# Optimization experiments

Hardware: AMD Instinct MI355X
Metric: run time of the kernel (lower is better)

## Reference

```python
import jax, jax.numpy as jnp
import numpy as np

B, N, A, H, MID = 256, 128, 15, 32, 256  # batch, nodes(=in_channels), actions, EQL-proxy hidden, critic mid_weight


def _glorot(k, shape):
    lim = float(np.sqrt(6.0 / (shape[0] + shape[1])))
    return jax.random.uniform(k, shape, jnp.float32, -lim, lim)


def setup_inputs() -> dict:
    key = jax.random.key(0)
    ks = jax.random.split(key, 10)
    obs = jax.random.normal(ks[0], (B, N), jnp.float32)
    return dict(
        obs=obs,
        # messenger EQL proxy: 4 -> H -> 1
        mw1=_glorot(ks[1], (4, H)), mb1=jnp.zeros((H,), jnp.float32),
        mw2=_glorot(ks[2], (H, 1)), mb2=jnp.zeros((1,), jnp.float32),
        # actor EQL proxy: 3 -> H -> 1
        aw1=_glorot(ks[3], (3, H)), ab1=jnp.zeros((H,), jnp.float32),
        aw2=_glorot(ks[4], (H, 1)), ab2=jnp.zeros((1,), jnp.float32),
        # critic MLP: N -> MID -> MID -> MID -> 1 (depth=4)
        cw1=_glorot(ks[5], (N, MID)), cb1=jnp.zeros((MID,), jnp.float32),
        cw2=_glorot(ks[6], (MID, MID)), cb2=jnp.zeros((MID,), jnp.float32),
        cw3=_glorot(ks[7], (MID, MID)), cb3=jnp.zeros((MID,), jnp.float32),
        cw4=_glorot(ks[8], (MID, 1)), cb4=jnp.zeros((1,), jnp.float32),
    )


def reference(obs, mw1, mb1, mw2, mb2, aw1, ab1, aw2, ab2,
              cw1, cb1, cw2, cb2, cw3, cb3, cw4, cb4):
    b, n = obs.shape
    coor = jnp.arange(n, dtype=jnp.float32) / n  # append_index coordinate channel
    x = jnp.stack([obs, jnp.broadcast_to(coor, obs.shape)], axis=-1)  # [B,n,2]

    # all-pairs message pass: msg_in[b,i,j] = concat(x[b,i], x[b,j])  -> [B,n,n,4]
    xi = jnp.broadcast_to(x[:, :, None, :], (b, n, n, 2))
    xj = jnp.broadcast_to(x[:, None, :, :], (b, n, n, 2))
    msg_in = jnp.concatenate([xi, xj], axis=-1)
    messages = jax.nn.relu(msg_in @ mw1 + mb1) @ mw2 + mb2  # [B,n,n,1]
    msg = jnp.sum(messages, axis=-2)[..., 0]  # sum over j, squeeze -> [B,n]

    # append_index again on the aggregated messages
    m = jnp.stack([msg, jnp.broadcast_to(coor, msg.shape)], axis=-1)  # [B,n,2]

    # node x action cross: am[b,i,a] = concat(m[b,i], a)  -> [B,n,A,3]
    acts = jnp.arange(A, dtype=jnp.float32)[None, None, :, None]
    mi = jnp.broadcast_to(m[:, :, None, :], (b, n, A, 2))
    aj = jnp.broadcast_to(acts, (b, n, A, 1))
    am = jnp.concatenate([mi, aj], axis=-1)
    am_messages = jax.nn.relu(am @ aw1 + ab1) @ aw2 + ab2  # [B,n,A,1]
    logits = jnp.sum(am_messages, axis=-3)[..., 0]  # sum over nodes (obs_dim=-3) -> [B,A]

    # critic MLP on raw obs
    h = jax.nn.relu(obs @ cw1 + cb1)
    h = jax.nn.relu(h @ cw2 + cb2)
    h = jax.nn.relu(h @ cw3 + cb3)
    value = h @ cw4 + cb4  # [B,1]
    return logits, value
```

## Files before the change

kernel.cpp:

```cpp
#include <hip/hip_runtime.h>

#define BB    256
#define NN    128
#define AA    15
#define HH    32
#define MIDD  256
#define NCRIT 16

typedef _Float16 h2_t  __attribute__((ext_vector_type(2)));
typedef _Float16 f16x8 __attribute__((ext_vector_type(8)));
typedef float    f32x4 __attribute__((ext_vector_type(4)));

struct MsgS {
    _Float16 vh[NN][HH];
    float4   p4[8][NN];
    float    part[4][16][8];
};
struct CriS {
    _Float16 hA[2][16][264];
};

__global__ __launch_bounds__(512, 4) void gacq_v13(
    const float* __restrict__ obs,
    const float* __restrict__ mw1, const float* __restrict__ mb1,
    const float* __restrict__ mw2, const float* __restrict__ mb2,
    const float* __restrict__ aw1, const float* __restrict__ ab1,
    const float* __restrict__ aw2, const float* __restrict__ ab2,
    const float* __restrict__ cw1, const float* __restrict__ cb1,
    const float* __restrict__ cw2, const float* __restrict__ cb2,
    const float* __restrict__ cw3, const float* __restrict__ cb3,
    const float* __restrict__ cw4, const float* __restrict__ cb4,
    float* __restrict__ out)
{
    __shared__ __align__(16) float aux_s[356];
    __shared__ __align__(16) float obs_s[NN];
    __shared__ __align__(16) union { MsgS m; CriS c; } u_s;

    const int blk  = blockIdx.x;
    const int t    = threadIdx.x;
    const int lane = t & 63;

    if (blk >= NCRIT) {
        const int b = blk - NCRIT;

        if (t < NN) obs_s[t] = obs[b * NN + t];
        if (t < 354) {
            float v;
            if      (t < 128) v = mw1[t];
            else if (t < 224) v = aw1[t - 128];
            else if (t < 256) v = ab1[t - 224];
            else if (t < 288) v = aw2[t - 256];
            else if (t < 320) v = mw2[t - 288];
            else if (t < 352) v = mb1[t - 320];
            else if (t == 352) v = mb2[0];
            else               v = ab2[0];
            aux_s[t] = v;
        }
        __syncthreads();

        for (int e = t; e < NN * HH / 2; e += 512) {
            const int   j  = e >> 4, kp = e & 15;
            const int   k0 = kp * 2;
            const float cj = (float)j * (1.0f / (float)NN);
            const float v0 = obs_s[j] * aux_s[64 + k0]     + cj * aux_s[96 + k0]     + aux_s[320 + k0];
            const float v1 = obs_s[j] * aux_s[64 + k0 + 1] + cj * aux_s[96 + k0 + 1] + aux_s[320 + k0 + 1];
            h2_t p; p[0] = (_Float16)v0; p[1] = (_Float16)v1;
            *(h2_t*)&u_s.m.vh[j][k0] = p;
        }

        const int kg = t & 7;
        const int rg = (t >> 3) & 15;
        const int jg = t >> 7;

        h2_t u2[8][2], w2h[2];
        w2h[0][0] = (_Float16)aux_s[288 + kg * 4 + 0];
        w2h[0][1] = (_Float16)aux_s[288 + kg * 4 + 1];
        w2h[1][0] = (_Float16)aux_s[288 + kg * 4 + 2];
        w2h[1][1] = (_Float16)aux_s[288 + kg * 4 + 3];
#pragma unroll
        for (int rr = 0; rr < 8; ++rr) {
            const int   row = rg * 8 + rr;
            const float ob  = obs_s[row];
            const float cr  = (float)row * (1.0f / (float)NN);
#pragma unroll
            for (int kp = 0; kp < 2; ++kp) {
                const int k0 = kg * 4 + kp * 2;
                u2[rr][kp][0] = (_Float16)(ob * aux_s[k0]     + cr * aux_s[32 + k0]);
                u2[rr][kp][1] = (_Float16)(ob * aux_s[k0 + 1] + cr * aux_s[32 + k0 + 1]);
            }
        }
        __syncthreads();

        float acc[8];
#pragma unroll
        for (int rr = 0; rr < 8; ++rr) acc[rr] = 0.f;
        const int j0 = jg * 32;
        {
            const h2_t   zero  = (h2_t)((_Float16)0);
            const uint2* vbase = (const uint2*)&u_s.m.vh[0][kg * 4];
            uint2 vc0 = vbase[j0 * 8];
            uint2 vc1 = vbase[(j0 + 1) * 8];
#pragma unroll 4
            for (int jj = 0; jj < 32; ++jj) {
                const int   nj = j0 + ((jj + 2) & 31);
                const uint2 vn = vbase[nj * 8];
                const h2_t  va = __builtin_bit_cast(h2_t, vc0.x);
                const h2_t  vb = __builtin_bit_cast(h2_t, vc0.y);
#pragma unroll
                for (int rr = 0; rr < 8; ++rr) {
                    h2_t s0 = u2[rr][0] + va;
                    h2_t s1 = u2[rr][1] + vb;
                    s0 = __builtin_elementwise_max(s0, zero);
                    s1 = __builtin_elementwise_max(s1, zero);
                    acc[rr] = __builtin_amdgcn_fdot2(s0, w2h[0], acc[rr], false);
                    acc[rr] = __builtin_amdgcn_fdot2(s1, w2h[1], acc[rr], false);
                }
                vc0 = vc1;
                vc1 = vn;
            }
        }
#pragma unroll
        for (int m = 1; m <= 4; m <<= 1)
#pragma unroll
            for (int rr = 0; rr < 8; ++rr) acc[rr] += __shfl_xor(acc[rr], m);
        if (kg == 0) {
            *(float4*)&u_s.m.part[jg][rg][0] = make_float4(acc[0], acc[1], acc[2], acc[3]);
            *(float4*)&u_s.m.part[jg][rg][4] = make_float4(acc[4], acc[5], acc[6], acc[7]);
        }
        __syncthreads();

        {
            const int row = t & 127;
            float mi = (float)NN * aux_s[352];
#pragma unroll
            for (int g = 0; g < 4; ++g) mi += u_s.m.part[g][row >> 3][row & 7];
            const float cr = (float)row * (1.0f / (float)NN);
#pragma unroll
            for (int it = 0; it < 2; ++it) {
                const int c  = (t >> 7) + it * 4;
                const int k0 = c * 4;
                float4 p;
                p.x = mi * aux_s[128 + k0 + 0] + cr * aux_s[160 + k0 + 0] + aux_s[224 + k0 + 0];
                p.y = mi * aux_s[128 + k0 + 1] + cr * aux_s[160 + k0 + 1] + aux_s[224 + k0 + 1];
                p.z = mi * aux_s[128 + k0 + 2] + cr * aux_s[160 + k0 + 2] + aux_s[224 + k0 + 2];
                p.w = mi * aux_s[128 + k0 + 3] + cr * aux_s[160 + k0 + 3] + aux_s[224 + k0 + 3];
                u_s.m.p4[c][row] = p;
            }
        }
        __syncthreads();

        {
            const int   a   = t >> 5;
            const int   sub = t & 31;
            const float fa  = (float)a;
            float qa[HH];
#pragma unroll
            for (int k = 0; k < HH; ++k) qa[k] = fa * aux_s[192 + k];
            float s0 = 0.f, s1 = 0.f, s2 = 0.f, s3 = 0.f;
#pragma unroll
            for (int m = 0; m < 4; ++m) {
                const int row = sub + 32 * m;
#pragma unroll
                for (int c = 0; c < 8; ++c) {
                    const float4 p4 = u_s.m.p4[c][row];
                    const float4 w4 = *(const float4*)&aux_s[256 + c * 4];
                    const int    k0 = c * 4;
                    s0 += fmaxf(p4.x + qa[k0 + 0], 0.f) * w4.x;
                    s1 += fmaxf(p4.y + qa[k0 + 1], 0.f) * w4.y;
                    s2 += fmaxf(p4.z + qa[k0 + 2], 0.f) * w4.z;
                    s3 += fmaxf(p4.w + qa[k0 + 3], 0.f) * w4.w;
                }
            }
            float s = (s0 + s1) + (s2 + s3);
#pragma unroll
            for (int off = 1; off < 32; off <<= 1) s += __shfl_xor(s, off);
            if (sub == 0 && a < AA)
                out[b * AA + a] = s + (float)NN * aux_s[353];
        }
    } else {
        const int b0 = blk * 16;

        for (int e = t; e < 16 * NN; e += 512)
            u_s.c.hA[0][e >> 7][e & 127] = (_Float16)obs[(b0 + (e >> 7)) * NN + (e & 127)];
        __syncthreads();

        const int w    = t >> 6;
        const int arow = lane & 15;
        const int koff = (lane >> 4) * 8;
        const int n0   = w * 32;

        auto critLayer = [&](const _Float16 (&Ain)[16][264], _Float16 (&Aout)[16][264],
                             const float* __restrict__ W, const float* __restrict__ bias,
                             const int Kd) {
            f32x4 acc0 = {0.f, 0.f, 0.f, 0.f};
            f32x4 acc1 = {0.f, 0.f, 0.f, 0.f};
            for (int ks = 0; ks < Kd; ks += 32) {
                const f16x8  af = *(const f16x8*)&Ain[arow][ks + koff];
                const float* wp = W + (size_t)(ks + koff) * MIDD + n0 + arow;
                f16x8 bf0, bf1;
#pragma unroll
                for (int j = 0; j < 8; ++j) {
                    bf0[j] = (_Float16)wp[j * MIDD];
                    bf1[j] = (_Float16)wp[j * MIDD + 16];
                }
                acc0 = __builtin_amdgcn_mfma_f32_16x16x32_f16(af, bf0, acc0, 0, 0, 0);
                acc1 = __builtin_amdgcn_mfma_f32_16x16x32_f16(af, bf1, acc1, 0, 0, 0);
            }
            const float b0v = bias[n0 + arow];
            const float b1v = bias[n0 + 16 + arow];
#pragma unroll
            for (int reg = 0; reg < 4; ++reg) {
                const int i = (lane >> 4) * 4 + reg;
                Aout[i][n0 + arow]      = (_Float16)fmaxf(acc0[reg] + b0v, 0.f);
                Aout[i][n0 + 16 + arow] = (_Float16)fmaxf(acc1[reg] + b1v, 0.f);
            }
        };

        critLayer(u_s.c.hA[0], u_s.c.hA[1], cw1, cb1, 128);
        __syncthreads();
        critLayer(u_s.c.hA[1], u_s.c.hA[0], cw2, cb2, 256);
        __syncthreads();
        critLayer(u_s.c.hA[0], u_s.c.hA[1], cw3, cb3, 256);
        __syncthreads();

        {
            const int i  = t >> 5;
            const int sl = t & 31;
            float s = 0.f;
#pragma unroll
            for (int j = 0; j < 8; ++j)
                s += (float)u_s.c.hA[1][i][sl * 8 + j] * cw4[sl * 8 + j];
#pragma unroll
            for (int off = 1; off < 32; off <<= 1) s += __shfl_xor(s, off);
            if (sl == 0) out[BB * AA + b0 + i] = s + cb4[0];
        }
    }
}

extern "C" void kernel_launch(void* const* d_in, const int* in_sizes, int n_in,
                              void* d_out, int out_size, void* d_ws, size_t ws_size,
                              hipStream_t stream) {
    const float* obs = (const float*)d_in[0];
    const float* mw1 = (const float*)d_in[1];
    const float* mb1 = (const float*)d_in[2];
    const float* mw2 = (const float*)d_in[3];
    const float* mb2 = (const float*)d_in[4];
    const float* aw1 = (const float*)d_in[5];
    const float* ab1 = (const float*)d_in[6];
    const float* aw2 = (const float*)d_in[7];
    const float* ab2 = (const float*)d_in[8];
    const float* cw1 = (const float*)d_in[9];
    const float* cb1 = (const float*)d_in[10];
    const float* cw2 = (const float*)d_in[11];
    const float* cb2 = (const float*)d_in[12];
    const float* cw3 = (const float*)d_in[13];
    const float* cb3 = (const float*)d_in[14];
    const float* cw4 = (const float*)d_in[15];
    const float* cb4 = (const float*)d_in[16];
    float* out = (float*)d_out;

    gacq_v13<<<dim3(BB + NCRIT), dim3(512), 0, stream>>>(
        obs, mw1, mb1, mw2, mb2, aw1, ab1, aw2, ab2,
        cw1, cb1, cw2, cb2, cw3, cb3, cw4, cb4, out);
}
```

Before: 17.25 us.

## Double block size to 1024 threads, splitting message j-loop across 8 groups

```diff
diff --git a/kernel.cpp b/kernel.cpp
--- a/kernel.cpp
+++ b/kernel.cpp
@@ -14,13 +14,13 @@
 struct MsgS {
     _Float16 vh[NN][HH];
     float4   p4[8][NN];
-    float    part[4][16][8];
+    float    part[8][16][8];
 };
 struct CriS {
     _Float16 hA[2][16][264];
 };
 
-__global__ __launch_bounds__(512, 4) void gacq_v13(
+__global__ __launch_bounds__(1024, 1) void gacq_v15(
     const float* __restrict__ obs,
     const float* __restrict__ mw1, const float* __restrict__ mb1,
     const float* __restrict__ mw2, const float* __restrict__ mb2,
@@ -44,21 +44,22 @@
         const int b = blk - NCRIT;
 
         if (t < NN) obs_s[t] = obs[b * NN + t];
-        if (t < 354) {
+        if (t >= 512 && t < 512 + 354) {
+            const int q = t - 512;
             float v;
-            if      (t < 128) v = mw1[t];
-            else if (t < 224) v = aw1[t - 128];
-            else if (t < 256) v = ab1[t - 224];
-            else if (t < 288) v = aw2[t - 256];
-            else if (t < 320) v = mw2[t - 288];
-            else if (t < 352) v = mb1[t - 320];
-            else if (t == 352) v = mb2[0];
+            if      (q < 128) v = mw1[q];
+            else if (q < 224) v = aw1[q - 128];
+            else if (q < 256) v = ab1[q - 224];
+            else if (q < 288) v = aw2[q - 256];
+            else if (q < 320) v = mw2[q - 288];
+            else if (q < 352) v = mb1[q - 320];
+            else if (q == 352) v = mb2[0];
             else               v = ab2[0];
-            aux_s[t] = v;
-        }
-        __syncthreads();
-
-        for (int e = t; e < NN * HH / 2; e += 512) {
+            aux_s[q] = v;
+        }
+        __syncthreads();
+
+        for (int e = t; e < NN * HH / 2; e += 1024) {
             const int   j  = e >> 4, kp = e & 15;
             const int   k0 = kp * 2;
             const float cj = (float)j * (1.0f / (float)NN);
@@ -94,15 +95,15 @@
         float acc[8];
 #pragma unroll
         for (int rr = 0; rr < 8; ++rr) acc[rr] = 0.f;
-        const int j0 = jg * 32;
+        const int j0 = jg * 16;
         {
             const h2_t   zero  = (h2_t)((_Float16)0);
             const uint2* vbase = (const uint2*)&u_s.m.vh[0][kg * 4];
             uint2 vc0 = vbase[j0 * 8];
             uint2 vc1 = vbase[(j0 + 1) * 8];
 #pragma unroll 4
-            for (int jj = 0; jj < 32; ++jj) {
-                const int   nj = j0 + ((jj + 2) & 31);
+            for (int jj = 0; jj < 16; ++jj) {
+                const int   nj = j0 + ((jj + 2) & 15);
                 const uint2 vn = vbase[nj * 8];
                 const h2_t  va = __builtin_bit_cast(h2_t, vc0.x);
                 const h2_t  vb = __builtin_bit_cast(h2_t, vc0.y);
@@ -129,11 +130,11 @@
         }
         __syncthreads();
 
-        {
+        if (t < 512) {
             const int row = t & 127;
             float mi = (float)NN * aux_s[352];
 #pragma unroll
-            for (int g = 0; g < 4; ++g) mi += u_s.m.part[g][row >> 3][row & 7];
+            for (int g = 0; g < 8; ++g) mi += u_s.m.part[g][row >> 3][row & 7];
             const float cr = (float)row * (1.0f / (float)NN);
 #pragma unroll
             for (int it = 0; it < 2; ++it) {
@@ -149,7 +150,7 @@
         }
         __syncthreads();
 
-        {
+        if (t < 512) {
             const int   a   = t >> 5;
             const int   sub = t & 31;
             const float fa  = (float)a;
@@ -180,14 +181,15 @@
     } else {
         const int b0 = blk * 16;
 
-        for (int e = t; e < 16 * NN; e += 512)
-            u_s.c.hA[0][e >> 7][e & 127] = (_Float16)obs[(b0 + (e >> 7)) * NN + (e & 127)];
+        if (t < 512)
+            for (int e = t; e < 16 * NN; e += 512)
+                u_s.c.hA[0][e >> 7][e & 127] = (_Float16)obs[(b0 + (e >> 7)) * NN + (e & 127)];
         __syncthreads();
 
         const int w    = t >> 6;
         const int arow = lane & 15;
         const int koff = (lane >> 4) * 8;
-        const int n0   = w * 32;
+        const int n0   = (w & 7) * 32;
 
         auto critLayer = [&](const _Float16 (&Ain)[16][264], _Float16 (&Aout)[16][264],
                              const float* __restrict__ W, const float* __restrict__ bias,
@@ -216,14 +218,14 @@
             }
         };
 
-        critLayer(u_s.c.hA[0], u_s.c.hA[1], cw1, cb1, 128);
-        __syncthreads();
-        critLayer(u_s.c.hA[1], u_s.c.hA[0], cw2, cb2, 256);
-        __syncthreads();
-        critLayer(u_s.c.hA[0], u_s.c.hA[1], cw3, cb3, 256);
-        __syncthreads();
-
-        {
+        if (t < 512) critLayer(u_s.c.hA[0], u_s.c.hA[1], cw1, cb1, 128);
+        __syncthreads();
+        if (t < 512) critLayer(u_s.c.hA[1], u_s.c.hA[0], cw2, cb2, 256);
+        __syncthreads();
+        if (t < 512) critLayer(u_s.c.hA[0], u_s.c.hA[1], cw3, cb3, 256);
+        __syncthreads();
+
+        if (t < 512) {
             const int i  = t >> 5;
             const int sl = t & 31;
             float s = 0.f;
@@ -259,7 +261,7 @@
     const float* cb4 = (const float*)d_in[16];
     float* out = (float*)d_out;
 
-    gacq_v13<<<dim3(BB + NCRIT), dim3(512), 0, stream>>>(
+    gacq_v15<<<dim3(BB + NCRIT), dim3(1024), 0, stream>>>(
         obs, mw1, mb1, mw2, mb2, aw1, ab1, aw2, ab2,
         cw1, cb1, cw2, cb2, cw3, cb3, cw4, cb4, out);
 }
```

Result: slower. 24.06 us (+39.5%).

## Split each batch's message rows across two blocks with atomic last-block reduction

Applied to the files above, without the earlier changes.

```diff
diff --git a/kernel.cpp b/kernel.cpp
--- a/kernel.cpp
+++ b/kernel.cpp
@@ -6,6 +6,8 @@
 #define HH    32
 #define MIDD  256
 #define NCRIT 16
+#define NMSG  (2 * BB)
+#define CTRF  8192
 
 typedef _Float16 h2_t  __attribute__((ext_vector_type(2)));
 typedef _Float16 f16x8 __attribute__((ext_vector_type(8)));
@@ -13,14 +15,14 @@
 
 struct MsgS {
     _Float16 vh[NN][HH];
-    float4   p4[8][NN];
-    float    part[4][16][8];
+    float4   p4[8][64];
+    float    part[8][8][8];
 };
 struct CriS {
     _Float16 hA[2][16][264];
 };
 
-__global__ __launch_bounds__(512, 4) void gacq_v13(
+__global__ __launch_bounds__(512, 4) void gacq_v16(
     const float* __restrict__ obs,
     const float* __restrict__ mw1, const float* __restrict__ mb1,
     const float* __restrict__ mw2, const float* __restrict__ mb2,
@@ -30,18 +32,21 @@
     const float* __restrict__ cw2, const float* __restrict__ cb2,
     const float* __restrict__ cw3, const float* __restrict__ cb3,
     const float* __restrict__ cw4, const float* __restrict__ cb4,
-    float* __restrict__ out)
+    float* __restrict__ out, float* __restrict__ wsf)
 {
     __shared__ __align__(16) float aux_s[356];
     __shared__ __align__(16) float obs_s[NN];
     __shared__ __align__(16) union { MsgS m; CriS c; } u_s;
+    __shared__ int last_s;
 
     const int blk  = blockIdx.x;
     const int t    = threadIdx.x;
     const int lane = t & 63;
 
     if (blk >= NCRIT) {
-        const int b = blk - NCRIT;
+        const int idx = blk - NCRIT;
+        const int b   = idx >> 1;
+        const int h   = idx & 1;
 
         if (t < NN) obs_s[t] = obs[b * NN + t];
         if (t < 354) {
@@ -69,8 +74,8 @@
         }
 
         const int kg = t & 7;
-        const int rg = (t >> 3) & 15;
-        const int jg = t >> 7;
+        const int rg = (t >> 3) & 7;
+        const int jg = t >> 6;
 
         h2_t u2[8][2], w2h[2];
         w2h[0][0] = (_Float16)aux_s[288 + kg * 4 + 0];
@@ -79,7 +84,7 @@
         w2h[1][1] = (_Float16)aux_s[288 + kg * 4 + 3];
 #pragma unroll
         for (int rr = 0; rr < 8; ++rr) {
-            const int   row = rg * 8 + rr;
+            const int   row = h * 64 + rg * 8 + rr;
             const float ob  = obs_s[row];
             const float cr  = (float)row * (1.0f / (float)NN);
 #pragma unroll
@@ -94,15 +99,15 @@
         float acc[8];
 #pragma unroll
         for (int rr = 0; rr < 8; ++rr) acc[rr] = 0.f;
-        const int j0 = jg * 32;
+        const int j0 = jg * 16;
         {
             const h2_t   zero  = (h2_t)((_Float16)0);
             const uint2* vbase = (const uint2*)&u_s.m.vh[0][kg * 4];
             uint2 vc0 = vbase[j0 * 8];
             uint2 vc1 = vbase[(j0 + 1) * 8];
 #pragma unroll 4
-            for (int jj = 0; jj < 32; ++jj) {
-                const int   nj = j0 + ((jj + 2) & 31);
+            for (int jj = 0; jj < 16; ++jj) {
+                const int   nj = j0 + ((jj + 2) & 15);
                 const uint2 vn = vbase[nj * 8];
                 const h2_t  va = __builtin_bit_cast(h2_t, vc0.x);
                 const h2_t  vb = __builtin_bit_cast(h2_t, vc0.y);
@@ -130,22 +135,20 @@
         __syncthreads();
 
         {
-            const int row = t & 127;
+            const int lr = t & 63;
+            const int c  = t >> 6;
             float mi = (float)NN * aux_s[352];
 #pragma unroll
-            for (int g = 0; g < 4; ++g) mi += u_s.m.part[g][row >> 3][row & 7];
-            const float cr = (float)row * (1.0f / (float)NN);
-#pragma unroll
-            for (int it = 0; it < 2; ++it) {
-                const int c  = (t >> 7) + it * 4;
-                const int k0 = c * 4;
-                float4 p;
-                p.x = mi * aux_s[128 + k0 + 0] + cr * aux_s[160 + k0 + 0] + aux_s[224 + k0 + 0];
-                p.y = mi * aux_s[128 + k0 + 1] + cr * aux_s[160 + k0 + 1] + aux_s[224 + k0 + 1];
-                p.z = mi * aux_s[128 + k0 + 2] + cr * aux_s[160 + k0 + 2] + aux_s[224 + k0 + 2];
-                p.w = mi * aux_s[128 + k0 + 3] + cr * aux_s[160 + k0 + 3] + aux_s[224 + k0 + 3];
-                u_s.m.p4[c][row] = p;
-            }
+            for (int g = 0; g < 8; ++g) mi += u_s.m.part[g][lr >> 3][lr & 7];
+            const int   row = h * 64 + lr;
+            const float cr  = (float)row * (1.0f / (float)NN);
+            const int   k0  = c * 4;
+            float4 p;
+            p.x = mi * aux_s[128 + k0 + 0] + cr * aux_s[160 + k0 + 0] + aux_s[224 + k0 + 0];
+            p.y = mi * aux_s[128 + k0 + 1] + cr * aux_s[160 + k0 + 1] + aux_s[224 + k0 + 1];
+            p.z = mi * aux_s[128 + k0 + 2] + cr * aux_s[160 + k0 + 2] + aux_s[224 + k0 + 2];
+            p.w = mi * aux_s[128 + k0 + 3] + cr * aux_s[160 + k0 + 3] + aux_s[224 + k0 + 3];
+            u_s.m.p4[c][lr] = p;
         }
         __syncthreads();
 
@@ -158,11 +161,11 @@
             for (int k = 0; k < HH; ++k) qa[k] = fa * aux_s[192 + k];
             float s0 = 0.f, s1 = 0.f, s2 = 0.f, s3 = 0.f;
 #pragma unroll
-            for (int m = 0; m < 4; ++m) {
-                const int row = sub + 32 * m;
+            for (int m = 0; m < 2; ++m) {
+                const int lr = sub + 32 * m;
 #pragma unroll
                 for (int c = 0; c < 8; ++c) {
-                    const float4 p4 = u_s.m.p4[c][row];
+                    const float4 p4 = u_s.m.p4[c][lr];
                     const float4 w4 = *(const float4*)&aux_s[256 + c * 4];
                     const int    k0 = c * 4;
                     s0 += fmaxf(p4.x + qa[k0 + 0], 0.f) * w4.x;
@@ -175,7 +178,30 @@
 #pragma unroll
             for (int off = 1; off < 32; off <<= 1) s += __shfl_xor(s, off);
             if (sub == 0 && a < AA)
-                out[b * AA + a] = s + (float)NN * aux_s[353];
+                __hip_atomic_store(&wsf[idx * 16 + a], s, __ATOMIC_RELAXED,
+                                   __HIP_MEMORY_SCOPE_AGENT);
+        }
+        __syncthreads();
+
+        if (t == 0) {
+            __threadfence();
+            int* ctr = (int*)&wsf[CTRF];
+            const int old = __hip_atomic_fetch_add(ctr, 1, __ATOMIC_ACQ_REL,
+                                                   __HIP_MEMORY_SCOPE_AGENT);
+            last_s = (old == NMSG - 1) ? 1 : 0;
+        }
+        __syncthreads();
+        if (last_s) {
+            const float ab2v = (float)NN * aux_s[353];
+            for (int i = t; i < BB * AA; i += 512) {
+                const int bb = i / AA;
+                const int aa = i - bb * AA;
+                const float pa = __hip_atomic_load(&wsf[(bb * 2 + 0) * 16 + aa],
+                                                   __ATOMIC_RELAXED, __HIP_MEMORY_SCOPE_AGENT);
+                const float pb = __hip_atomic_load(&wsf[(bb * 2 + 1) * 16 + aa],
+                                                   __ATOMIC_RELAXED, __HIP_MEMORY_SCOPE_AGENT);
+                out[i] = pa + pb + ab2v;
+            }
         }
     } else {
         const int b0 = blk * 16;
@@ -258,8 +284,11 @@
     const float* cw4 = (const float*)d_in[15];
     const float* cb4 = (const float*)d_in[16];
     float* out = (float*)d_out;
-
-    gacq_v13<<<dim3(BB + NCRIT), dim3(512), 0, stream>>>(
+    float* wsf = (float*)d_ws;
+
+    hipMemsetAsync((char*)d_ws + CTRF * sizeof(float), 0, sizeof(int), stream);
+
+    gacq_v16<<<dim3(NCRIT + NMSG), dim3(512), 0, stream>>>(
         obs, mw1, mb1, mw2, mb2, aw1, ab1, aw2, ab2,
-        cw1, cb1, cw2, cb2, cw3, cb3, cw4, cb4, out);
+        cw1, cb1, cw2, cb2, cw3, cb3, cw4, cb4, out, wsf);
 }
```

Result: slower. 38.16 us (+121.2%).
